# Optimization experiments

Hardware: AMD Instinct MI355X
Metric: run time of the kernel (lower is better)

## Reference

```python
import jax, jax.numpy as jnp
import numpy as np

H = 8
HD = 64
RHO = 0.1


def setup_inputs() -> dict:
    key = jax.random.key(0)
    ks = jax.random.split(key, 5)
    B, L, D = 4, 512, 512
    x = jax.random.normal(ks[0], (B, L, D), dtype=jnp.float32)
    # store projection weights as [in, out] so y = x @ W (equivalent to torch Linear with W.T)
    Wq = jax.random.normal(ks[1], (D, H * HD), dtype=jnp.float32) * 0.02
    Wk = jax.random.normal(ks[2], (D, H * HD), dtype=jnp.float32) * 0.02
    Wv = jax.random.normal(ks[3], (D, H * HD), dtype=jnp.float32) * 0.02
    Wo = jax.random.normal(ks[4], (H * HD, D), dtype=jnp.float32) * 0.02
    return {"x": x, "Wq": Wq, "Wk": Wk, "Wv": Wv, "Wo": Wo}


def _build_adjacency(S):
    # S: [B, H, L, L]. A = (1/L) sum_j [thresholded outer(S[:,:,:,j]) / HD with zero diag]
    B, Hn, L, _ = S.shape
    eye = jnp.eye(L, dtype=bool)
    S_cols = jnp.transpose(S, (3, 0, 1, 2))  # [L, B, H, L]

    def step(acc, s_col):
        # s_col: [B, H, L]; U_j[i,k] = s_col[i] * s_col[k] / HD
        U = s_col[..., :, None] * s_col[..., None, :] / HD  # [B,H,L,L]
        U = jnp.where(eye, 0.0, U)
        A_j = jnp.where(U > RHO, U, 0.0)
        return acc + A_j, None

    A_sum, _ = jax.lax.scan(step, jnp.zeros_like(S), S_cols)
    return A_sum / L


def _normalize_adjacency(A):
    L = A.shape[-1]
    A_tilde = A + jnp.eye(L, dtype=A.dtype)
    D = jnp.clip(A_tilde.sum(axis=-1, keepdims=True), 1e-6, None)
    D_inv_sqrt = D ** -0.5  # [B,H,L,1]
    return D_inv_sqrt * A_tilde * jnp.swapaxes(D_inv_sqrt, -1, -2)


def reference(x, Wq, Wk, Wv, Wo):
    B, L, D = x.shape
    scale = jnp.sqrt(jnp.asarray(HD, dtype=x.dtype))
    def proj(W):
        return jnp.einsum('bld,de->ble', x, W).reshape(B, L, H, HD).transpose(0, 2, 1, 3)
    Q, K, V = proj(Wq), proj(Wk), proj(Wv)  # [B,H,L,HD]
    S = jnp.einsum('bhid,bhjd->bhij', Q, K)  # [B,H,L,L]
    A = _build_adjacency(S)
    A_hat = _normalize_adjacency(A)
    # jump: Phi(S) = A_hat @ S @ A_hat^T
    S_jump = jnp.einsum('bhij,bhjk,bhlk->bhil', A_hat, S, A_hat) / scale
    attn = jax.nn.softmax(S_jump, axis=-1)
    out = jnp.einsum('bhij,bhjd->bhid', attn, V)  # [B,H,L,HD]
    out = out.transpose(0, 2, 1, 3).reshape(B, L, H * HD)
    return jnp.einsum('ble,ed->bld', out, Wo)
```

## Files before the change

kernel.cpp:

```cpp
#include <hip/hip_runtime.h>
#include <math.h>


typedef __attribute__((ext_vector_type(8))) short short8v;
typedef __attribute__((ext_vector_type(4))) float f32x4;
typedef _Float16 h2 __attribute__((ext_vector_type(2)));

__device__ __forceinline__ void split8(const float* v, unsigned* hi, unsigned* lo)
{
    #pragma unroll
    for (int q = 0; q < 4; ++q) {
        const unsigned b0 = __float_as_uint(v[2 * q])     & 0xFFFF0000u;
        const unsigned b1 = __float_as_uint(v[2 * q + 1]) & 0xFFFF0000u;
        const float d0 = v[2 * q]     - __uint_as_float(b0);
        const float d1 = v[2 * q + 1] - __uint_as_float(b1);
        hi[q] = (b0 >> 16) | b1;
        lo[q] = (__float_as_uint(d0) >> 16) | (__float_as_uint(d1) & 0xFFFF0000u);
    }
}

template<int BT>
__global__ __launch_bounds__(256)
void gemm_mfma(const float* __restrict__ Ap, const float* __restrict__ Bp,
               float* __restrict__ Cp, int K, int lda, int ldb, int ldc,
               long sA, long sB, long sC, float scale)
{
    const float* __restrict__ A = Ap + (long)blockIdx.z * sA;
    const float* __restrict__ B = Bp + (long)blockIdx.z * sB;
    float* __restrict__ C = Cp + (long)blockIdx.z * sC;
    const int m0 = blockIdx.y << 7, n0 = blockIdx.x << 7;

    __shared__ short Ah[128 * 32], Al[128 * 32], Bh[128 * 32], Bl[128 * 32];

    const int tid = threadIdx.x;
    const int lane = tid & 63, wv = tid >> 6;
    const int wr = wv >> 1, wc = wv & 1;

    f32x4 acc[4][4] = {};

    for (int k0 = 0; k0 < K; k0 += 32) {
        {
            const int row = tid >> 1;
            const int swz = (row & 3) ^ ((row >> 2) & 3);
            #pragma unroll
            for (int gg = 0; gg < 2; ++gg) {
                const int g = ((tid & 1) << 1) + gg;
                const float* src = A + (long)(m0 + row) * lda + k0 + (g << 3);
                float v[8];
                *(float4*)&v[0] = *(const float4*)src;
                *(float4*)&v[4] = *(const float4*)(src + 4);
                unsigned hi[4], lo[4];
                split8(v, hi, lo);
                const int off = row * 32 + ((g ^ swz) << 3);
                *(uint4*)&Ah[off] = *(uint4*)hi;
                *(uint4*)&Al[off] = *(uint4*)lo;
            }
        }
        if (BT) {
            const int row = tid >> 1;
            const int swz = (row & 3) ^ ((row >> 2) & 3);
            #pragma unroll
            for (int gg = 0; gg < 2; ++gg) {
                const int g = ((tid & 1) << 1) + gg;
                const float* src = B + (long)(n0 + row) * ldb + k0 + (g << 3);
                float v[8];
                *(float4*)&v[0] = *(const float4*)src;
                *(float4*)&v[4] = *(const float4*)(src + 4);
                unsigned hi[4], lo[4];
                split8(v, hi, lo);
                const int off = row * 32 + ((g ^ swz) << 3);
                *(uint4*)&Bh[off] = *(uint4*)hi;
                *(uint4*)&Bl[off] = *(uint4*)lo;
            }
        } else {
            const int n = tid & 127;
            const int swz = (n & 3) ^ ((n >> 2) & 3);
            #pragma unroll
            for (int gg = 0; gg < 2; ++gg) {
                const int g = ((tid >> 7) << 1) + gg;
                float v[8];
                #pragma unroll
                for (int e = 0; e < 8; ++e)
                    v[e] = B[(long)(k0 + (g << 3) + e) * ldb + n0 + n];
                unsigned hi[4], lo[4];
                split8(v, hi, lo);
                const int off = n * 32 + ((g ^ swz) << 3);
                *(uint4*)&Bh[off] = *(uint4*)hi;
                *(uint4*)&Bl[off] = *(uint4*)lo;
            }
        }
        __syncthreads();

        {
            const int r = lane & 15, g = lane >> 4;
            const int lswz = (r & 3) ^ ((r >> 2) & 3);
            const int gslot = ((g ^ lswz) << 3);
            const int abase = ((wr << 6) + r) * 32 + gslot;
            const int bbase = ((wc << 6) + r) * 32 + gslot;
            short8v afh[4], afl[4], bfh[4], bfl[4];
            #pragma unroll
            for (int f = 0; f < 4; ++f) {
                afh[f] = *(short8v*)&Ah[abase + f * 512];
                afl[f] = *(short8v*)&Al[abase + f * 512];
                bfh[f] = *(short8v*)&Bh[bbase + f * 512];
                bfl[f] = *(short8v*)&Bl[bbase + f * 512];
            }
            #pragma unroll
            for (int fi = 0; fi < 4; ++fi)
                #pragma unroll
                for (int fj = 0; fj < 4; ++fj) {
                    acc[fi][fj] = __builtin_amdgcn_mfma_f32_16x16x32_bf16(
                        afh[fi], bfh[fj], acc[fi][fj], 0, 0, 0);
                    acc[fi][fj] = __builtin_amdgcn_mfma_f32_16x16x32_bf16(
                        afh[fi], bfl[fj], acc[fi][fj], 0, 0, 0);
                    acc[fi][fj] = __builtin_amdgcn_mfma_f32_16x16x32_bf16(
                        afl[fi], bfh[fj], acc[fi][fj], 0, 0, 0);
                }
        }
        __syncthreads();
    }

    const int r = lane & 15, g = lane >> 4;
    #pragma unroll
    for (int fi = 0; fi < 4; ++fi) {
        const int gr0 = m0 + (wr << 6) + fi * 16 + g * 4;
        #pragma unroll
        for (int fj = 0; fj < 4; ++fj) {
            const int gc = n0 + (wc << 6) + fj * 16 + r;
            #pragma unroll
            for (int qq = 0; qq < 4; ++qq)
                C[(long)(gr0 + qq) * ldc + gc] = acc[fi][fj][qq] * scale;
        }
    }
}

__global__ __launch_bounds__(256)
void gemm_qkv_mfma(const float* __restrict__ x, const float* __restrict__ Wq,
                   const float* __restrict__ Wk, const float* __restrict__ Wv,
                   float* __restrict__ QKV)
{
    const int m0 = blockIdx.y << 7;
    const int ng = blockIdx.x << 7;
    const float* __restrict__ W = (ng < 512) ? Wq : (ng < 1024) ? Wk : Wv;
    const int n0 = ng & 511;
    float* __restrict__ C = QKV + (long)(ng >> 9) * (1 << 20);

    __shared__ short Ah[128 * 32], Al[128 * 32], Bh[128 * 32], Bl[128 * 32];

    const int tid = threadIdx.x;
    const int lane = tid & 63, wv = tid >> 6;
    const int wr = wv >> 1, wc = wv & 1;

    f32x4 acc[4][4] = {};

    for (int k0 = 0; k0 < 512; k0 += 32) {
        {
            const int row = tid >> 1;
            const int swz = (row & 3) ^ ((row >> 2) & 3);
            #pragma unroll
            for (int gg = 0; gg < 2; ++gg) {
                const int g = ((tid & 1) << 1) + gg;
                const float* src = x + (long)(m0 + row) * 512 + k0 + (g << 3);
                float v[8];
                *(float4*)&v[0] = *(const float4*)src;
                *(float4*)&v[4] = *(const float4*)(src + 4);
                unsigned hi[4], lo[4];
                split8(v, hi, lo);
                const int off = row * 32 + ((g ^ swz) << 3);
                *(uint4*)&Ah[off] = *(uint4*)hi;
                *(uint4*)&Al[off] = *(uint4*)lo;
            }
        }
        {
            const int n = tid & 127;
            const int swz = (n & 3) ^ ((n >> 2) & 3);
            #pragma unroll
            for (int gg = 0; gg < 2; ++gg) {
                const int g = ((tid >> 7) << 1) + gg;
                float v[8];
                #pragma unroll
                for (int e = 0; e < 8; ++e)
                    v[e] = W[(long)(k0 + (g << 3) + e) * 512 + n0 + n];
                unsigned hi[4], lo[4];
                split8(v, hi, lo);
                const int off = n * 32 + ((g ^ swz) << 3);
                *(uint4*)&Bh[off] = *(uint4*)hi;
                *(uint4*)&Bl[off] = *(uint4*)lo;
            }
        }
        __syncthreads();

        {
            const int r = lane & 15, g = lane >> 4;
            const int lswz = (r & 3) ^ ((r >> 2) & 3);
            const int gslot = ((g ^ lswz) << 3);
            const int abase = ((wr << 6) + r) * 32 + gslot;
            const int bbase = ((wc << 6) + r) * 32 + gslot;
            short8v afh[4], afl[4], bfh[4], bfl[4];
            #pragma unroll
            for (int f = 0; f < 4; ++f) {
                afh[f] = *(short8v*)&Ah[abase + f * 512];
                afl[f] = *(short8v*)&Al[abase + f * 512];
                bfh[f] = *(short8v*)&Bh[bbase + f * 512];
                bfl[f] = *(short8v*)&Bl[bbase + f * 512];
            }
            #pragma unroll
            for (int fi = 0; fi < 4; ++fi)
                #pragma unroll
                for (int fj = 0; fj < 4; ++fj) {
                    acc[fi][fj] = __builtin_amdgcn_mfma_f32_16x16x32_bf16(
                        afh[fi], bfh[fj], acc[fi][fj], 0, 0, 0);
                    acc[fi][fj] = __builtin_amdgcn_mfma_f32_16x16x32_bf16(
                        afh[fi], bfl[fj], acc[fi][fj], 0, 0, 0);
                    acc[fi][fj] = __builtin_amdgcn_mfma_f32_16x16x32_bf16(
                        afl[fi], bfh[fj], acc[fi][fj], 0, 0, 0);
                }
        }
        __syncthreads();
    }

    const int r = lane & 15, g = lane >> 4;
    #pragma unroll
    for (int fi = 0; fi < 4; ++fi) {
        const int gr0 = m0 + (wr << 6) + fi * 16 + g * 4;
        #pragma unroll
        for (int fj = 0; fj < 4; ++fj) {
            const int nl = n0 + (wc << 6) + fj * 16 + r;
            const int h = nl >> 6, d = nl & 63;
            #pragma unroll
            for (int qq = 0; qq < 4; ++qq) {
                const int m = gr0 + qq;
                const int b = m >> 9, l = m & 511;
                C[((long)((b * 8 + h) * 512 + l)) * 64 + d] = acc[fi][fj][qq];
            }
        }
    }
}

__global__ __launch_bounds__(256)
void adj_kernel(const float* __restrict__ S, float* __restrict__ A)
{
    const int bh = blockIdx.y;
    const float* __restrict__ Sh = S + (long)bh * 262144;
    float* __restrict__ Ah = A + (long)bh * 262144;

    int ti = 0, rem = blockIdx.x;
    while (rem >= 8 - ti) { rem -= 8 - ti; ++ti; }
    const int tk = ti + rem;
    const int i0 = ti << 6, k0 = tk << 6;

    __shared__ __align__(16) char smem_raw[17408];

    const int tid  = threadIdx.x;
    const int lane = tid & 63;
    const int wv   = tid >> 6;
    const int ly8  = (lane >> 3) << 3;
    const int lx8  = (lane & 7) << 3;
    const int r4   = lane >> 2;
    const int q    = lane & 3;

    h2 (*stgL)[68] = (h2(*)[68])(smem_raw + wv * 4352);
    h2 (*stgR)[68] = (h2(*)[68])(smem_raw + wv * 4352 + 2176);

    const h2 nC2  = { (_Float16)(-6.4f), (_Float16)(-6.4f) };
    const h2 z2   = { (_Float16)0.0f,    (_Float16)0.0f };
    const h2 big2 = { (_Float16)32768.0f,(_Float16)32768.0f };
    const h2 c2   = { (_Float16)6.4f,    (_Float16)6.4f };

    h2 acc2[8][8];
    #pragma unroll
    for (int i = 0; i < 8; ++i)
        #pragma unroll
        for (int j = 0; j < 8; ++j)
            acc2[i][j] = z2;

    const int jw = wv << 7;
    for (int c = 0; c < 8; ++c) {
        const int j0 = jw + (c << 4);
        float4 rl[4], rr[4];
        #pragma unroll
        for (int p = 0; p < 4; ++p) {
            rl[p] = *(const float4*)(Sh + (long)(i0 + r4 + (p << 4)) * 512 + j0 + (q << 2));
            rr[p] = *(const float4*)(Sh + (long)(k0 + r4 + (p << 4)) * 512 + j0 + (q << 2));
        }
        #pragma unroll
        for (int p = 0; p < 4; ++p) {
            const int row = r4 + (p << 4);
            h2 h0, h1;
            h0[0] = (_Float16)rl[p].x; h0[1] = (_Float16)rl[p].y;
            h1[0] = (_Float16)rl[p].z; h1[1] = (_Float16)rl[p].w;
            stgL[(q << 1) + 0][row] = h0;
            stgL[(q << 1) + 1][row] = h1;
            h0[0] = (_Float16)rr[p].x; h0[1] = (_Float16)rr[p].y;
            h1[0] = (_Float16)rr[p].z; h1[1] = (_Float16)rr[p].w;
            stgR[(q << 1) + 0][row] = h0;
            stgR[(q << 1) + 1][row] = h1;
        }
        __builtin_amdgcn_s_waitcnt(0);
        #pragma unroll
        for (int jp = 0; jp < 8; ++jp) {
            h2 a2[8], b2[8];
            *(uint4*)&a2[0] = *(const uint4*)&stgL[jp][ly8];
            *(uint4*)&a2[4] = *(const uint4*)&stgL[jp][ly8 + 4];
            *(uint4*)&b2[0] = *(const uint4*)&stgR[jp][lx8];
            *(uint4*)&b2[4] = *(const uint4*)&stgR[jp][lx8 + 4];
            #pragma unroll
            for (int i = 0; i < 8; ++i)
                #pragma unroll
                for (int j = 0; j < 8; ++j) {
                    const h2 d = a2[i] * b2[j] + nC2;
                    const h2 t = __builtin_elementwise_max(d, z2);
                    const h2 m = __builtin_elementwise_min(t * big2 + t, t + c2);
                    acc2[i][j] += m;
                }
        }
    }

    float* buf0 = (float*)smem_raw;
    float* buf1 = (float*)(smem_raw + 4352);
    float  f[8][8];

    #pragma unroll
    for (int qp = 0; qp < 4; ++qp) {
        float v[16];
        #pragma unroll
        for (int e = 0; e < 16; ++e) {
            const h2 hh = acc2[(qp << 1) + (e >> 3)][e & 7];
            v[e] = (float)hh[0] + (float)hh[1];
        }
        __syncthreads();
        if (wv == 1 || wv == 2) {
            float* dst = (wv == 1 ? buf0 : buf1) + lane * 17;
            #pragma unroll
            for (int e = 0; e < 16; ++e) dst[e] = v[e];
        }
        __syncthreads();
        if (wv == 0 || wv == 3) {
            const float* src = (wv == 0 ? buf0 : buf1) + lane * 17;
            #pragma unroll
            for (int e = 0; e < 16; ++e) v[e] += src[e];
        }
        __syncthreads();
        if (wv == 3) {
            float* dst = buf0 + lane * 17;
            #pragma unroll
            for (int e = 0; e < 16; ++e) dst[e] = v[e];
        }
        __syncthreads();
        if (wv == 0) {
            const float* src = buf0 + lane * 17;
            #pragma unroll
            for (int e = 0; e < 16; ++e)
                f[(qp << 1) + (e >> 3)][e & 7] = v[e] + src[e];
        }
    }

    if (wv == 0) {
        const float SC = 1.0f / 32768.0f;
        #pragma unroll
        for (int i = 0; i < 8; ++i)
            #pragma unroll
            for (int j = 0; j < 8; ++j)
                f[i][j] *= SC;
        if (ti == tk) {
            #pragma unroll
            for (int i = 0; i < 8; ++i)
                #pragma unroll
                for (int j = 0; j < 8; ++j)
                    if (ly8 + i == lx8 + j) f[i][j] = 0.0f;
        }
        #pragma unroll
        for (int i = 0; i < 8; ++i) {
            float* dst = Ah + (long)(i0 + ly8 + i) * 512 + k0 + lx8;
            *(float4*)dst       = make_float4(f[i][0], f[i][1], f[i][2], f[i][3]);
            *(float4*)(dst + 4) = make_float4(f[i][4], f[i][5], f[i][6], f[i][7]);
        }
        if (ti != tk) {
            #pragma unroll
            for (int j = 0; j < 8; ++j) {
                float* dst = Ah + (long)(k0 + lx8 + j) * 512 + i0 + ly8;
                *(float4*)dst       = make_float4(f[0][j], f[1][j], f[2][j], f[3][j]);
                *(float4*)(dst + 4) = make_float4(f[4][j], f[5][j], f[6][j], f[7][j]);
            }
        }
    }
}

__global__ __launch_bounds__(256)
void rowsum_kernel(const float* __restrict__ A, float* __restrict__ R)
{
    const int row = (blockIdx.x << 2) + (threadIdx.x >> 6);
    const int lane = threadIdx.x & 63;
    const float* p = A + (long)row * 512;
    float s = 0.0f;
    #pragma unroll
    for (int t = 0; t < 8; ++t) s += p[lane + (t << 6)];
    #pragma unroll
    for (int off = 32; off; off >>= 1) s += __shfl_xor(s, off, 64);
    if (lane == 0) R[row] = 1.0f / sqrtf(fmaxf(1.0f + s, 1e-6f));
}

__global__ __launch_bounds__(256)
void ahat_kernel(float* __restrict__ A, const float* __restrict__ R)
{
    const long i4 = ((long)blockIdx.x * 256 + threadIdx.x) << 2;
    const long off = i4 & 262143;
    const long bh = i4 >> 18;
    const int i = (int)(off >> 9);
    const int k = (int)(off & 511);
    const float ri = R[(bh << 9) + i];
    const float* Rk = R + (bh << 9) + k;
    float4 v = *(float4*)(A + i4);
    v.x = ri * Rk[0] * (v.x + ((k + 0) == i ? 1.0f : 0.0f));
    v.y = ri * Rk[1] * (v.y + ((k + 1) == i ? 1.0f : 0.0f));
    v.z = ri * Rk[2] * (v.z + ((k + 2) == i ? 1.0f : 0.0f));
    v.w = ri * Rk[3] * (v.w + ((k + 3) == i ? 1.0f : 0.0f));
    *(float4*)(A + i4) = v;
}

__global__ __launch_bounds__(256)
void softmax_kernel(float* __restrict__ P)
{
    const int row = (blockIdx.x << 2) + (threadIdx.x >> 6);
    const int lane = threadIdx.x & 63;
    float* p = P + (long)row * 512 + (lane << 3);
    float4 v0 = *(float4*)p;
    float4 v1 = *(float4*)(p + 4);
    float mx = fmaxf(fmaxf(fmaxf(v0.x, v0.y), fmaxf(v0.z, v0.w)),
                     fmaxf(fmaxf(v1.x, v1.y), fmaxf(v1.z, v1.w)));
    #pragma unroll
    for (int off = 32; off; off >>= 1) mx = fmaxf(mx, __shfl_xor(mx, off, 64));
    float e[8];
    e[0] = __expf(v0.x - mx); e[1] = __expf(v0.y - mx);
    e[2] = __expf(v0.z - mx); e[3] = __expf(v0.w - mx);
    e[4] = __expf(v1.x - mx); e[5] = __expf(v1.y - mx);
    e[6] = __expf(v1.z - mx); e[7] = __expf(v1.w - mx);
    float s = (((e[0] + e[1]) + (e[2] + e[3])) + ((e[4] + e[5]) + (e[6] + e[7])));
    #pragma unroll
    for (int off = 32; off; off >>= 1) s += __shfl_xor(s, off, 64);
    const float inv = 1.0f / s;
    *(float4*)p       = make_float4(e[0] * inv, e[1] * inv, e[2] * inv, e[3] * inv);
    *(float4*)(p + 4) = make_float4(e[4] * inv, e[5] * inv, e[6] * inv, e[7] * inv);
}

__global__ __launch_bounds__(256)
void gemm_pv_mfma(const float* __restrict__ P, const float* __restrict__ V,
                  float* __restrict__ Of)
{
    const int bh = blockIdx.z;
    const float* __restrict__ Pp = P + (long)bh * 262144;
    const float* __restrict__ Vp = V + (long)bh * 32768;
    const int bb = bh >> 3, hh = bh & 7;
    const int m0 = blockIdx.y << 7;

    __shared__ short Ph[128 * 32], Pl[128 * 32], Vh[64 * 32], Vl[64 * 32];

    const int tid = threadIdx.x;
    const int lane = tid & 63, wv = tid >> 6;

    f32x4 acc[2][4] = {};

    for (int k0 = 0; k0 < 512; k0 += 32) {
        {
            const int row = tid >> 1;
            const int swz = (row & 3) ^ ((row >> 2) & 3);
            #pragma unroll
            for (int gg = 0; gg < 2; ++gg) {
                const int g = ((tid & 1) << 1) + gg;
                const float* src = Pp + (long)(m0 + row) * 512 + k0 + (g << 3);
                float v[8];
                *(float4*)&v[0] = *(const float4*)src;
                *(float4*)&v[4] = *(const float4*)(src + 4);
                unsigned hi[4], lo[4];
                split8(v, hi, lo);
                const int off = row * 32 + ((g ^ swz) << 3);
                *(uint4*)&Ph[off] = *(uint4*)hi;
                *(uint4*)&Pl[off] = *(uint4*)lo;
            }
        }
        {
            const int n = tid & 63, g = tid >> 6;
            const int swz = (n & 3) ^ ((n >> 2) & 3);
            float v[8];
            #pragma unroll
            for (int e = 0; e < 8; ++e)
                v[e] = Vp[(long)(k0 + (g << 3) + e) * 64 + n];
            unsigned hi[4], lo[4];
            split8(v, hi, lo);
            const int off = n * 32 + ((g ^ swz) << 3);
            *(uint4*)&Vh[off] = *(uint4*)hi;
            *(uint4*)&Vl[off] = *(uint4*)lo;
        }
        __syncthreads();

        {
            const int r = lane & 15, g = lane >> 4;
            const int lswz = (r & 3) ^ ((r >> 2) & 3);
            const int gslot = ((g ^ lswz) << 3);
            short8v afh[2], afl[2], bfh[4], bfl[4];
            #pragma unroll
            for (int fi = 0; fi < 2; ++fi) {
                const int abase = ((wv << 5) + (fi << 4) + r) * 32 + gslot;
                afh[fi] = *(short8v*)&Ph[abase];
                afl[fi] = *(short8v*)&Pl[abase];
            }
            #pragma unroll
            for (int fj = 0; fj < 4; ++fj) {
                const int bbase = ((fj << 4) + r) * 32 + gslot;
                bfh[fj] = *(short8v*)&Vh[bbase];
                bfl[fj] = *(short8v*)&Vl[bbase];
            }
            #pragma unroll
            for (int fi = 0; fi < 2; ++fi)
                #pragma unroll
                for (int fj = 0; fj < 4; ++fj) {
                    acc[fi][fj] = __builtin_amdgcn_mfma_f32_16x16x32_bf16(
                        afh[fi], bfh[fj], acc[fi][fj], 0, 0, 0);
                    acc[fi][fj] = __builtin_amdgcn_mfma_f32_16x16x32_bf16(
                        afh[fi], bfl[fj], acc[fi][fj], 0, 0, 0);
                    acc[fi][fj] = __builtin_amdgcn_mfma_f32_16x16x32_bf16(
                        afl[fi], bfh[fj], acc[fi][fj], 0, 0, 0);
                }
        }
        __syncthreads();
    }

    const int r = lane & 15, g = lane >> 4;
    #pragma unroll
    for (int fi = 0; fi < 2; ++fi) {
        const int l0 = m0 + (wv << 5) + fi * 16 + g * 4;
        #pragma unroll
        for (int fj = 0; fj < 4; ++fj) {
            const int d = fj * 16 + r;
            #pragma unroll
            for (int qq = 0; qq < 4; ++qq)
                Of[((long)((bb << 9) + l0 + qq) << 9) + (hh << 6) + d] = acc[fi][fj][qq];
        }
    }
}

extern "C" void kernel_launch(void* const* d_in, const int* in_sizes, int n_in,
                              void* d_out, int out_size, void* d_ws, size_t ws_size,
                              hipStream_t stream)
{
    const float* x  = (const float*)d_in[0];
    const float* Wq = (const float*)d_in[1];
    const float* Wk = (const float*)d_in[2];
    const float* Wv = (const float*)d_in[3];
    const float* Wo = (const float*)d_in[4];
    float* out = (float*)d_out;

    float* ws = (float*)d_ws;
    float* Q  = ws;
    float* Kt = Q  + (1u << 20);
    float* V  = Kt + (1u << 20);
    float* S  = V  + (1u << 20);
    float* Am = S  + (8u << 20);
    float* T  = Am + (8u << 20);
    float* R  = T  + (8u << 20);

    dim3 blk(256);

    gemm_qkv_mfma<<<dim3(12, 16, 1), blk, 0, stream>>>(x, Wq, Wk, Wv, Q);

    gemm_mfma<1><<<dim3(4, 4, 32), blk, 0, stream>>>(Q, Kt, S, 64, 64, 64, 512,
                                                     32768, 32768, 262144, 1.0f);

    adj_kernel<<<dim3(36, 32), blk, 0, stream>>>(S, Am);

    rowsum_kernel<<<dim3(4096), blk, 0, stream>>>(Am, R);

    ahat_kernel<<<dim3(8192), blk, 0, stream>>>(Am, R);

    gemm_mfma<0><<<dim3(4, 4, 32), blk, 0, stream>>>(Am, S, T, 512, 512, 512, 512,
                                                     262144, 262144, 262144, 1.0f);

    gemm_mfma<1><<<dim3(4, 4, 32), blk, 0, stream>>>(T, Am, S, 512, 512, 512, 512,
                                                     262144, 262144, 262144, 0.125f);

    softmax_kernel<<<dim3(4096), blk, 0, stream>>>(S);

    gemm_pv_mfma<<<dim3(1, 4, 32), blk, 0, stream>>>(S, V, Q);

    gemm_mfma<0><<<dim3(4, 16, 1), blk, 0, stream>>>(Q, Wo, out, 512, 512, 512, 512,
                                                     0, 0, 0, 1.0f);
}
```

Before: 439.1 us.

## Split adjacency reduction over j into two partial buffers and prefetch S loads

The adjacency kernel now splits the j (summation) dimension across two grid slices, doubling the block count from 1152 to 2304. Each slice writes its own partial buffer, reusing the T scratch as the second one. Rowsum and normalization then read and add both partials. Each chunk's global loads are issued before the current chunk's compute, with a waitcnt that covers only LDS traffic, and launch bounds request higher occupancy. The aim is to fill the GPU better and hide load latency, at the cost of an extra 32 MB partial write and read.

Result: faster. 416.3 us (-5.2%).

```diff
diff --git a/kernel.cpp b/kernel.cpp
--- a/kernel.cpp
+++ b/kernel.cpp
@@ -237,12 +237,14 @@
     }
 }
 
-__global__ __launch_bounds__(256)
-void adj_kernel(const float* __restrict__ S, float* __restrict__ A)
-{
-    const int bh = blockIdx.y;
+__global__ __launch_bounds__(256, 4)
+void adj_kernel(const float* __restrict__ S, float* __restrict__ P0,
+                float* __restrict__ P1)
+{
+    const int bh = blockIdx.z;
     const float* __restrict__ Sh = S + (long)bh * 262144;
-    float* __restrict__ Ah = A + (long)bh * 262144;
+    float* __restrict__ Ph = ((blockIdx.y == 0) ? P0 : P1) + (long)bh * 262144;
+    const int jbase = blockIdx.y << 8;
 
     int ti = 0, rem = blockIdx.x;
     while (rem >= 8 - ti) { rem -= 8 - ti; ++ti; }
@@ -274,15 +276,18 @@
         for (int j = 0; j < 8; ++j)
             acc2[i][j] = z2;
 
-    const int jw = wv << 7;
-    for (int c = 0; c < 8; ++c) {
-        const int j0 = jw + (c << 4);
-        float4 rl[4], rr[4];
-        #pragma unroll
-        for (int p = 0; p < 4; ++p) {
-            rl[p] = *(const float4*)(Sh + (long)(i0 + r4 + (p << 4)) * 512 + j0 + (q << 2));
-            rr[p] = *(const float4*)(Sh + (long)(k0 + r4 + (p << 4)) * 512 + j0 + (q << 2));
-        }
+    const int jw = jbase + (wv << 6);
+    const float* srcL = Sh + (long)(i0 + r4) * 512 + jw + (q << 2);
+    const float* srcR = Sh + (long)(k0 + r4) * 512 + jw + (q << 2);
+
+    float4 rl[4], rr[4];
+    #pragma unroll
+    for (int p = 0; p < 4; ++p) {
+        rl[p] = *(const float4*)(srcL + (long)(p << 4) * 512);
+        rr[p] = *(const float4*)(srcR + (long)(p << 4) * 512);
+    }
+
+    for (int c = 0; c < 4; ++c) {
         #pragma unroll
         for (int p = 0; p < 4; ++p) {
             const int row = r4 + (p << 4);
@@ -296,7 +301,16 @@
             stgR[(q << 1) + 0][row] = h0;
             stgR[(q << 1) + 1][row] = h1;
         }
-        __builtin_amdgcn_s_waitcnt(0);
+        if (c < 3) {
+            const int joff = (c + 1) << 4;
+            #pragma unroll
+            for (int p = 0; p < 4; ++p) {
+                rl[p] = *(const float4*)(srcL + (long)(p << 4) * 512 + joff);
+                rr[p] = *(const float4*)(srcR + (long)(p << 4) * 512 + joff);
+            }
+        }
+        asm volatile("s_waitcnt lgkmcnt(0)" ::: "memory");
+        __builtin_amdgcn_sched_barrier(0);
         #pragma unroll
         for (int jp = 0; jp < 8; ++jp) {
             h2 a2[8], b2[8];
@@ -371,14 +385,14 @@
         }
         #pragma unroll
         for (int i = 0; i < 8; ++i) {
-            float* dst = Ah + (long)(i0 + ly8 + i) * 512 + k0 + lx8;
+            float* dst = Ph + (long)(i0 + ly8 + i) * 512 + k0 + lx8;
             *(float4*)dst       = make_float4(f[i][0], f[i][1], f[i][2], f[i][3]);
             *(float4*)(dst + 4) = make_float4(f[i][4], f[i][5], f[i][6], f[i][7]);
         }
         if (ti != tk) {
             #pragma unroll
             for (int j = 0; j < 8; ++j) {
-                float* dst = Ah + (long)(k0 + lx8 + j) * 512 + i0 + ly8;
+                float* dst = Ph + (long)(k0 + lx8 + j) * 512 + i0 + ly8;
                 *(float4*)dst       = make_float4(f[0][j], f[1][j], f[2][j], f[3][j]);
                 *(float4*)(dst + 4) = make_float4(f[4][j], f[5][j], f[6][j], f[7][j]);
             }
@@ -387,21 +401,24 @@
 }
 
 __global__ __launch_bounds__(256)
-void rowsum_kernel(const float* __restrict__ A, float* __restrict__ R)
+void rowsum_kernel(const float* __restrict__ P0, const float* __restrict__ P1,
+                   float* __restrict__ R)
 {
     const int row = (blockIdx.x << 2) + (threadIdx.x >> 6);
     const int lane = threadIdx.x & 63;
-    const float* p = A + (long)row * 512;
+    const float* p0 = P0 + (long)row * 512;
+    const float* p1 = P1 + (long)row * 512;
     float s = 0.0f;
     #pragma unroll
-    for (int t = 0; t < 8; ++t) s += p[lane + (t << 6)];
+    for (int t = 0; t < 8; ++t) s += p0[lane + (t << 6)] + p1[lane + (t << 6)];
     #pragma unroll
     for (int off = 32; off; off >>= 1) s += __shfl_xor(s, off, 64);
     if (lane == 0) R[row] = 1.0f / sqrtf(fmaxf(1.0f + s, 1e-6f));
 }
 
 __global__ __launch_bounds__(256)
-void ahat_kernel(float* __restrict__ A, const float* __restrict__ R)
+void ahat_kernel(float* __restrict__ P0, const float* __restrict__ P1,
+                 const float* __restrict__ R)
 {
     const long i4 = ((long)blockIdx.x * 256 + threadIdx.x) << 2;
     const long off = i4 & 262143;
@@ -410,12 +427,13 @@
     const int k = (int)(off & 511);
     const float ri = R[(bh << 9) + i];
     const float* Rk = R + (bh << 9) + k;
-    float4 v = *(float4*)(A + i4);
-    v.x = ri * Rk[0] * (v.x + ((k + 0) == i ? 1.0f : 0.0f));
-    v.y = ri * Rk[1] * (v.y + ((k + 1) == i ? 1.0f : 0.0f));
-    v.z = ri * Rk[2] * (v.z + ((k + 2) == i ? 1.0f : 0.0f));
-    v.w = ri * Rk[3] * (v.w + ((k + 3) == i ? 1.0f : 0.0f));
-    *(float4*)(A + i4) = v;
+    float4 v0 = *(float4*)(P0 + i4);
+    float4 v1 = *(const float4*)(P1 + i4);
+    v0.x = ri * Rk[0] * ((v0.x + v1.x) + ((k + 0) == i ? 1.0f : 0.0f));
+    v0.y = ri * Rk[1] * ((v0.y + v1.y) + ((k + 1) == i ? 1.0f : 0.0f));
+    v0.z = ri * Rk[2] * ((v0.z + v1.z) + ((k + 2) == i ? 1.0f : 0.0f));
+    v0.w = ri * Rk[3] * ((v0.w + v1.w) + ((k + 3) == i ? 1.0f : 0.0f));
+    *(float4*)(P0 + i4) = v0;
 }
 
 __global__ __launch_bounds__(256)
@@ -566,11 +584,11 @@
     gemm_mfma<1><<<dim3(4, 4, 32), blk, 0, stream>>>(Q, Kt, S, 64, 64, 64, 512,
                                                      32768, 32768, 262144, 1.0f);
 
-    adj_kernel<<<dim3(36, 32), blk, 0, stream>>>(S, Am);
-
-    rowsum_kernel<<<dim3(4096), blk, 0, stream>>>(Am, R);
-
-    ahat_kernel<<<dim3(8192), blk, 0, stream>>>(Am, R);
+    adj_kernel<<<dim3(36, 2, 32), blk, 0, stream>>>(S, Am, T);
+
+    rowsum_kernel<<<dim3(4096), blk, 0, stream>>>(Am, T, R);
+
+    ahat_kernel<<<dim3(8192), blk, 0, stream>>>(Am, T, R);
 
     gemm_mfma<0><<<dim3(4, 4, 32), blk, 0, stream>>>(Am, S, T, 512, 512, 512, 512,
                                                      262144, 262144, 262144, 1.0f);
```
